# Performance work log

Measured on AMD Instinct MI355X. Metric: run time of the kernel, lower is better.

The kernel has to match this reference:

```python
import jax, jax.numpy as jnp
import numpy as np
from jax import lax

LSTM_UNITS = 64
BATCH = 2048
TIMESTEPS = 1024


def _lstm_cell(x, h, c, W_ih, W_hh, b_ih, b_hh):
    # PyTorch LSTMCell gate order: i, f, g, o
    gates = x @ W_ih.T + b_ih + h @ W_hh.T + b_hh
    i, f, g, o = jnp.split(gates, 4, axis=-1)
    c_new = jax.nn.sigmoid(f) * c + jax.nn.sigmoid(i) * jnp.tanh(g)
    h_new = jax.nn.sigmoid(o) * jnp.tanh(c_new)
    return h_new, c_new


def setup_inputs() -> dict:
    key = jax.random.key(0)
    ks = jax.random.split(key, 9)
    U = LSTM_UNITS
    s0 = 1.0 / np.sqrt(U)  # torch LSTMCell init scale (hidden=64)
    s1 = 1.0  # hidden=1 -> scale 1/sqrt(1)
    inp = {
        "input": jax.random.normal(ks[0], (BATCH, TIMESTEPS), dtype=jnp.float32),
        # c0: LSTMCell(1, 64)
        "W_ih0": jax.random.uniform(ks[1], (4 * U, 1), jnp.float32, -s0, s0),
        "W_hh0": jax.random.uniform(ks[2], (4 * U, U), jnp.float32, -s0, s0),
        "b_ih0": jax.random.uniform(ks[3], (4 * U,), jnp.float32, -s0, s0),
        "b_hh0": jax.random.uniform(ks[4], (4 * U,), jnp.float32, -s0, s0),
        # c1: LSTMCell(64, 1)
        "W_ih1": jax.random.uniform(ks[5], (4, U), jnp.float32, -s1, s1),
        "W_hh1": jax.random.uniform(ks[6], (4, 1), jnp.float32, -s1, s1),
        "b_ih1": jax.random.uniform(ks[7], (4,), jnp.float32, -s1, s1),
        "b_hh1": jax.random.uniform(ks[8], (4,), jnp.float32, -s1, s1),
    }
    return inp


def reference(input, W_ih0, W_hh0, b_ih0, b_hh0, W_ih1, W_hh1, b_ih1, b_hh1):
    B = input.shape[0]
    U = LSTM_UNITS
    dt = input.dtype
    h0 = jnp.zeros((B, U), dt)
    c0 = jnp.zeros((B, U), dt)
    h1 = jnp.zeros((B, 1), dt)
    c1 = jnp.zeros((B, 1), dt)

    def step(carry, x_t):
        h0, c0, h1, c1 = carry
        h0n, c0n = _lstm_cell(x_t, h0, c0, W_ih0, W_hh0, b_ih0, b_hh0)
        # NOTE: the original feeds the CELL state c0n (not h0n) into layer 2
        h1n, c1n = _lstm_cell(c0n, h1, c1, W_ih1, W_hh1, b_ih1, b_hh1)
        # output per step is the cell state of layer 2
        return (h0n, c0n, h1n, c1n), c1n

    xs = input.T[:, :, None]  # (T, B, 1)
    _, ys = lax.scan(step, (h0, c0, h1, c1), xs)  # ys: (T, B, 1)
    return ys[:, :, 0].T  # (B, T)
```

## Files before the change

kernel.cpp:

```cpp
#include <hip/hip_runtime.h>

#define T_STEPS 1024
#define BATCH 2048
#define BTILE 8
#define HS 36

typedef short short8 __attribute__((ext_vector_type(8)));
typedef float f32x4 __attribute__((ext_vector_type(4)));
typedef float f32x2 __attribute__((ext_vector_type(2)));

__device__ __forceinline__ float fast_rcp(float x) {
#if __has_builtin(__builtin_amdgcn_rcpf)
    return __builtin_amdgcn_rcpf(x);
#else
    return 1.0f / x;
#endif
}

__device__ __forceinline__ float fast_exp2(float x) {
#if __has_builtin(__builtin_amdgcn_exp2f)
    return __builtin_amdgcn_exp2f(x);
#else
    return exp2f(x);
#endif
}

__device__ __forceinline__ float sigf(float x) {
    return fast_rcp(1.0f + fast_exp2(-1.44269504f * x));
}

__device__ __forceinline__ f32x2 sigf2(f32x2 v) {
    f32x2 t = v * (-1.44269504f);
    f32x2 e = {fast_exp2(t[0]), fast_exp2(t[1])};
    e = e + 1.0f;
    return f32x2{fast_rcp(e[0]), fast_rcp(e[1])};
}

__device__ __forceinline__ float tanh_fast(float x) {
    float e = fast_exp2(2.88539008f * x);
    return 1.0f - 2.0f * fast_rcp(e + 1.0f);
}

__device__ __forceinline__ f32x2 tanh2(f32x2 v) {
    f32x2 t = v * 2.88539008f;
    f32x2 e = {fast_exp2(t[0]), fast_exp2(t[1])};
    e = e + 1.0f;
    f32x2 r = {fast_rcp(e[0]), fast_rcp(e[1])};
    return f32x2{1.0f, 1.0f} - 2.0f * r;
}

__device__ __forceinline__ unsigned f2bf(float x) {
    unsigned u = __float_as_uint(x);
    unsigned r = u + 0x7FFFu + ((u >> 16) & 1u);
    return r >> 16;
}
__device__ __forceinline__ float bf2f(unsigned b) {
    return __uint_as_float(b << 16);
}

__device__ __forceinline__ unsigned cvt_pk_bf16(float a, float b) {
    unsigned r;
    asm("v_cvt_pk_bf16_f32 %0, %1, %2" : "=v"(r) : "v"(a), "v"(b));
    return r;
}

__device__ __forceinline__ void step_barrier() {
    asm volatile("s_waitcnt lgkmcnt(0)\n\ts_barrier" ::: "memory");
}

__global__ __launch_bounds__(320, 1)
void lstm_v16_kernel(const float* __restrict__ input,
                     const float* __restrict__ W_ih0,
                     const float* __restrict__ W_hh0,
                     const float* __restrict__ b_ih0,
                     const float* __restrict__ b_hh0,
                     const float* __restrict__ W_ih1,
                     const float* __restrict__ W_hh1,
                     const float* __restrict__ b_ih1,
                     const float* __restrict__ b_hh1,
                     float* __restrict__ out)
{
    const int tid = threadIdx.x;
    const int w8  = tid >> 6;
    const int l   = tid & 63;
    const int q16 = l >> 4;
    const int n16 = l & 15;
    const int n8  = l & 7;
    const int hi8 = n16 >> 3;
    const int ua  = 16 * w8 + 4 * q16 + 2 * hi8;
    const int bbase = blockIdx.x * BTILE;

    __shared__ __align__(16) unsigned Hbuf[2][3][16][HS];
    __shared__ float Xb[2][BTILE][65];

    for (int i = tid; i < 2 * 3 * 16 * HS; i += 320)
        reinterpret_cast<unsigned*>(Hbuf)[i] = 0u;

    short8 a1[4][2];
    f32x2 wg2[4], bg2[4];
    if (w8 < 4) {
        #pragma unroll
        for (int g = 0; g < 4; ++g) {
            #pragma unroll
            for (int kt = 0; kt < 2; ++kt) {
                const float* p = W_hh0 + (size_t)(16 * (w8 + 4 * g) + n16) * 64 + kt * 32 + q16 * 8;
                short8 a;
                #pragma unroll
                for (int j = 0; j < 8; ++j) a[j] = (short)f2bf(p[j]);
                a1[g][kt] = a;
            }
        }
        #pragma unroll
        for (int g = 0; g < 4; ++g) {
            int rA = g * 64 + ua;
            int rB = rA + 1;
            wg2[g] = f32x2{W_ih0[rA], W_ih0[rB]};
            bg2[g] = f32x2{b_ih0[rA] + b_hh0[rA], b_ih0[rB] + b_hh0[rB]};
        }
    }

    short8 a2h[2], a2l[2];
    float wh1[4], bb1[4];
    if (w8 == 4) {
        #pragma unroll
        for (int kt = 0; kt < 2; ++kt) {
            short8 ah = {0,0,0,0,0,0,0,0}, al = {0,0,0,0,0,0,0,0};
            if (n16 < 4) {
                const float* p = W_ih1 + (size_t)n16 * 64 + kt * 32 + q16 * 8;
                #pragma unroll
                for (int j = 0; j < 8; ++j) {
                    unsigned hb = f2bf(p[j]);
                    ah[j] = (short)hb;
                    al[j] = (short)f2bf(p[j] - bf2f(hb));
                }
            }
            a2h[kt] = ah; a2l[kt] = al;
        }
        #pragma unroll
        for (int g = 0; g < 4; ++g) { wh1[g] = W_hh1[g]; bb1[g] = b_ih1[g] + b_hh1[g]; }
    }

    const int xr = (tid >> 5) & 7;
    const int xc = tid & 31;
    const float* rowptr = input + (size_t)(bbase + xr) * T_STEPS;
    if (tid < 256) {
        Xb[0][xr][xc]      = rowptr[xc];
        Xb[0][xr][xc + 32] = rowptr[xc + 32];
    }
    float xnA = 0.0f, xnB = 0.0f;
    f32x2 c02 = {0.0f, 0.0f};
    float h1 = 0.0f, c1 = 0.0f;

    __syncthreads();

    int par = 0;
    #pragma unroll 2
    for (int t = 0; t < T_STEPS; ++t) {
        if (w8 < 4) {
            if ((t & 63) == 0 && t + 64 < T_STEPS) {
                xnA = rowptr[t + 64 + xc];
                xnB = rowptr[t + 64 + xc + 32];
            }
            const int cp = (t >> 6) & 1;

            const unsigned* Hrow = &Hbuf[par][0][n16][0];
            short8 hb0 = *reinterpret_cast<const short8*>(Hrow + 4 * q16);
            short8 hb1 = *reinterpret_cast<const short8*>(Hrow + 16 + 4 * q16);

            f32x4 accv[4];
            #pragma unroll
            for (int g = 0; g < 4; ++g) {
                f32x4 z = {0.0f, 0.0f, 0.0f, 0.0f};
                z = __builtin_amdgcn_mfma_f32_16x16x32_bf16(a1[g][0], hb0, z, 0, 0, 0);
                z = __builtin_amdgcn_mfma_f32_16x16x32_bf16(a1[g][1], hb1, z, 0, 0, 0);
                accv[g] = z;
            }

            float vA[4], vB[4];
            #pragma unroll
            for (int g = 0; g < 4; ++g) {
                int pa = __float_as_int(accv[g][0]);
                pa = __builtin_amdgcn_update_dpp(pa, __float_as_int(accv[g][2]), 0x118, 0xf, 0xC, false);
                int pb = __float_as_int(accv[g][1]);
                pb = __builtin_amdgcn_update_dpp(pb, __float_as_int(accv[g][3]), 0x118, 0xf, 0xC, false);
                vA[g] = __int_as_float(pa);
                vB[g] = __int_as_float(pb);
            }

            float x = Xb[cp][n8][t & 63];
            f32x2 xx = {x, x};
            f32x2 gi = f32x2{vA[0], vB[0]} + (xx * wg2[0] + bg2[0]);
            f32x2 gf = f32x2{vA[1], vB[1]} + (xx * wg2[1] + bg2[1]);
            f32x2 gg = f32x2{vA[2], vB[2]} + (xx * wg2[2] + bg2[2]);
            f32x2 go = f32x2{vA[3], vB[3]} + (xx * wg2[3] + bg2[3]);

            f32x2 si = sigf2(gi);
            f32x2 sf = sigf2(gf);
            f32x2 tg = tanh2(gg);
            f32x2 c0n2 = sf * c02 + si * tg;
            c02 = c0n2;
            f32x2 so = sigf2(go);
            f32x2 th = tanh2(c0n2);
            f32x2 h0n2 = so * th;

            const int widx = 8 * w8 + 2 * q16 + hi8;
            unsigned hword  = cvt_pk_bf16(h0n2[0], h0n2[1]);
            Hbuf[par ^ 1][0][n8][widx] = hword;
            unsigned chword = cvt_pk_bf16(c0n2[0], c0n2[1]);
            float hiA = bf2f(chword & 0xFFFFu);
            float hiB = bf2f(chword >> 16);
            f32x2 lo = c0n2 - f32x2{hiA, hiB};
            unsigned clword = cvt_pk_bf16(lo[0], lo[1]);
            Hbuf[par ^ 1][1][n8][widx] = chword;
            Hbuf[par ^ 1][2][n8][widx] = clword;

            if ((t & 63) == 63 && t + 1 < T_STEPS) {
                Xb[cp ^ 1][xr][xc]      = xnA;
                Xb[cp ^ 1][xr][xc + 32] = xnB;
            }
        } else {
            if (t > 0) {
                const unsigned* Ch = &Hbuf[par][1][n16][0];
                const unsigned* Cl = &Hbuf[par][2][n16][0];
                short8 ch0 = *reinterpret_cast<const short8*>(Ch + 4 * q16);
                short8 ch1 = *reinterpret_cast<const short8*>(Ch + 16 + 4 * q16);
                short8 cl0 = *reinterpret_cast<const short8*>(Cl + 4 * q16);
                short8 cl1 = *reinterpret_cast<const short8*>(Cl + 16 + 4 * q16);
                f32x4 zA = {0.0f, 0.0f, 0.0f, 0.0f};
                f32x4 zB = {0.0f, 0.0f, 0.0f, 0.0f};
                zA = __builtin_amdgcn_mfma_f32_16x16x32_bf16(a2h[0], ch0, zA, 0, 0, 0);
                zB = __builtin_amdgcn_mfma_f32_16x16x32_bf16(a2l[1], ch1, zB, 0, 0, 0);
                zA = __builtin_amdgcn_mfma_f32_16x16x32_bf16(a2h[1], ch1, zA, 0, 0, 0);
                zB = __builtin_amdgcn_mfma_f32_16x16x32_bf16(a2h[0], cl0, zB, 0, 0, 0);
                zA = __builtin_amdgcn_mfma_f32_16x16x32_bf16(a2l[0], ch0, zA, 0, 0, 0);
                zB = __builtin_amdgcn_mfma_f32_16x16x32_bf16(a2h[1], cl1, zB, 0, 0, 0);
                f32x4 z = zA + zB;
                if (l < 8) {
                    float gi = z[0] + bb1[0] + h1 * wh1[0];
                    float gf = z[1] + bb1[1] + h1 * wh1[1];
                    float gg = z[2] + bb1[2] + h1 * wh1[2];
                    float go = z[3] + bb1[3] + h1 * wh1[3];
                    float c1n = sigf(gf) * c1 + sigf(gi) * tanh_fast(gg);
                    c1 = c1n;
                    h1 = sigf(go) * tanh_fast(c1n);
                    out[(size_t)(bbase + l) * T_STEPS + (t - 1)] = c1n;
                }
            }
        }

        step_barrier();
        par ^= 1;
    }

    if (w8 == 4) {
        const unsigned* Ch = &Hbuf[par][1][n16][0];
        const unsigned* Cl = &Hbuf[par][2][n16][0];
        short8 ch0 = *reinterpret_cast<const short8*>(Ch + 4 * q16);
        short8 ch1 = *reinterpret_cast<const short8*>(Ch + 16 + 4 * q16);
        short8 cl0 = *reinterpret_cast<const short8*>(Cl + 4 * q16);
        short8 cl1 = *reinterpret_cast<const short8*>(Cl + 16 + 4 * q16);
        f32x4 zA = {0.0f, 0.0f, 0.0f, 0.0f};
        f32x4 zB = {0.0f, 0.0f, 0.0f, 0.0f};
        zA = __builtin_amdgcn_mfma_f32_16x16x32_bf16(a2h[0], ch0, zA, 0, 0, 0);
        zB = __builtin_amdgcn_mfma_f32_16x16x32_bf16(a2l[1], ch1, zB, 0, 0, 0);
        zA = __builtin_amdgcn_mfma_f32_16x16x32_bf16(a2h[1], ch1, zA, 0, 0, 0);
        zB = __builtin_amdgcn_mfma_f32_16x16x32_bf16(a2h[0], cl0, zB, 0, 0, 0);
        zA = __builtin_amdgcn_mfma_f32_16x16x32_bf16(a2l[0], ch0, zA, 0, 0, 0);
        zB = __builtin_amdgcn_mfma_f32_16x16x32_bf16(a2h[1], cl1, zB, 0, 0, 0);
        f32x4 z = zA + zB;
        if (l < 8) {
            float gi = z[0] + bb1[0] + h1 * wh1[0];
            float gf = z[1] + bb1[1] + h1 * wh1[1];
            float gg = z[2] + bb1[2] + h1 * wh1[2];
            float c1n = sigf(gf) * c1 + sigf(gi) * tanh_fast(gg);
            out[(size_t)(bbase + l) * T_STEPS + (T_STEPS - 1)] = c1n;
        }
    }
}

extern "C" void kernel_launch(void* const* d_in, const int* in_sizes, int n_in,
                              void* d_out, int out_size, void* d_ws, size_t ws_size,
                              hipStream_t stream) {
    const float* input = (const float*)d_in[0];
    const float* W_ih0 = (const float*)d_in[1];
    const float* W_hh0 = (const float*)d_in[2];
    const float* b_ih0 = (const float*)d_in[3];
    const float* b_hh0 = (const float*)d_in[4];
    const float* W_ih1 = (const float*)d_in[5];
    const float* W_hh1 = (const float*)d_in[6];
    const float* b_ih1 = (const float*)d_in[7];
    const float* b_hh1 = (const float*)d_in[8];
    float* out = (float*)d_out;

    lstm_v16_kernel<<<dim3(BATCH / BTILE), dim3(320), 0, stream>>>(
        input, W_ih0, W_hh0, b_ih0, b_hh0, W_ih1, W_hh1, b_ih1, b_hh1, out);
}
```

Before: 473.6 us.

## Defer layer-2 cell-state packing to next step and split MFMA accumulation chain

```diff
diff --git a/kernel.cpp b/kernel.cpp
--- a/kernel.cpp
+++ b/kernel.cpp
@@ -69,7 +69,7 @@
 }
 
 __global__ __launch_bounds__(320, 1)
-void lstm_v16_kernel(const float* __restrict__ input,
+void lstm_v18_kernel(const float* __restrict__ input,
                      const float* __restrict__ W_ih0,
                      const float* __restrict__ W_hh0,
                      const float* __restrict__ b_ih0,
@@ -88,6 +88,7 @@
     const int n8  = l & 7;
     const int hi8 = n16 >> 3;
     const int ua  = 16 * w8 + 4 * q16 + 2 * hi8;
+    const int widx = 8 * w8 + 2 * q16 + hi8;
     const int bbase = blockIdx.x * BTILE;
 
     __shared__ __align__(16) unsigned Hbuf[2][3][16][HS];
@@ -149,6 +150,7 @@
     }
     float xnA = 0.0f, xnB = 0.0f;
     f32x2 c02 = {0.0f, 0.0f};
+    f32x2 c_sv = {0.0f, 0.0f};
     float h1 = 0.0f, c1 = 0.0f;
 
     __syncthreads();
@@ -157,6 +159,16 @@
     #pragma unroll 2
     for (int t = 0; t < T_STEPS; ++t) {
         if (w8 < 4) {
+            if (t > 0) {
+                unsigned chword = cvt_pk_bf16(c_sv[0], c_sv[1]);
+                float hiA = bf2f(chword & 0xFFFFu);
+                float hiB = bf2f(chword >> 16);
+                f32x2 lo = c_sv - f32x2{hiA, hiB};
+                unsigned clword = cvt_pk_bf16(lo[0], lo[1]);
+                Hbuf[par ^ 1][1][n8][widx] = chword;
+                Hbuf[par ^ 1][2][n8][widx] = clword;
+            }
+
             if ((t & 63) == 0 && t + 64 < T_STEPS) {
                 xnA = rowptr[t + 64 + xc];
                 xnB = rowptr[t + 64 + xc + 32];
@@ -170,10 +182,10 @@
             f32x4 accv[4];
             #pragma unroll
             for (int g = 0; g < 4; ++g) {
-                f32x4 z = {0.0f, 0.0f, 0.0f, 0.0f};
-                z = __builtin_amdgcn_mfma_f32_16x16x32_bf16(a1[g][0], hb0, z, 0, 0, 0);
-                z = __builtin_amdgcn_mfma_f32_16x16x32_bf16(a1[g][1], hb1, z, 0, 0, 0);
-                accv[g] = z;
+                f32x4 zz = {0.0f, 0.0f, 0.0f, 0.0f};
+                f32x4 z0 = __builtin_amdgcn_mfma_f32_16x16x32_bf16(a1[g][0], hb0, zz, 0, 0, 0);
+                f32x4 z1 = __builtin_amdgcn_mfma_f32_16x16x32_bf16(a1[g][1], hb1, zz, 0, 0, 0);
+                accv[g] = z0 + z1;
             }
 
             float vA[4], vB[4];
@@ -203,23 +215,15 @@
             f32x2 th = tanh2(c0n2);
             f32x2 h0n2 = so * th;
 
-            const int widx = 8 * w8 + 2 * q16 + hi8;
-            unsigned hword  = cvt_pk_bf16(h0n2[0], h0n2[1]);
-            Hbuf[par ^ 1][0][n8][widx] = hword;
-            unsigned chword = cvt_pk_bf16(c0n2[0], c0n2[1]);
-            float hiA = bf2f(chword & 0xFFFFu);
-            float hiB = bf2f(chword >> 16);
-            f32x2 lo = c0n2 - f32x2{hiA, hiB};
-            unsigned clword = cvt_pk_bf16(lo[0], lo[1]);
-            Hbuf[par ^ 1][1][n8][widx] = chword;
-            Hbuf[par ^ 1][2][n8][widx] = clword;
+            Hbuf[par ^ 1][0][n8][widx] = cvt_pk_bf16(h0n2[0], h0n2[1]);
+            c_sv = c0n2;
 
             if ((t & 63) == 63 && t + 1 < T_STEPS) {
                 Xb[cp ^ 1][xr][xc]      = xnA;
                 Xb[cp ^ 1][xr][xc + 32] = xnB;
             }
         } else {
-            if (t > 0) {
+            if (t > 1) {
                 const unsigned* Ch = &Hbuf[par][1][n16][0];
                 const unsigned* Cl = &Hbuf[par][2][n16][0];
                 short8 ch0 = *reinterpret_cast<const short8*>(Ch + 4 * q16);
@@ -243,7 +247,7 @@
                     float c1n = sigf(gf) * c1 + sigf(gi) * tanh_fast(gg);
                     c1 = c1n;
                     h1 = sigf(go) * tanh_fast(c1n);
-                    out[(size_t)(bbase + l) * T_STEPS + (t - 1)] = c1n;
+                    out[(size_t)(bbase + l) * T_STEPS + (t - 2)] = c1n;
                 }
             }
         }
@@ -252,28 +256,45 @@
         par ^= 1;
     }
 
+    if (w8 < 4) {
+        unsigned chword = cvt_pk_bf16(c_sv[0], c_sv[1]);
+        float hiA = bf2f(chword & 0xFFFFu);
+        float hiB = bf2f(chword >> 16);
+        f32x2 lo = c_sv - f32x2{hiA, hiB};
+        unsigned clword = cvt_pk_bf16(lo[0], lo[1]);
+        Hbuf[1][1][n8][widx] = chword;
+        Hbuf[1][2][n8][widx] = clword;
+    }
+    step_barrier();
+
     if (w8 == 4) {
-        const unsigned* Ch = &Hbuf[par][1][n16][0];
-        const unsigned* Cl = &Hbuf[par][2][n16][0];
-        short8 ch0 = *reinterpret_cast<const short8*>(Ch + 4 * q16);
-        short8 ch1 = *reinterpret_cast<const short8*>(Ch + 16 + 4 * q16);
-        short8 cl0 = *reinterpret_cast<const short8*>(Cl + 4 * q16);
-        short8 cl1 = *reinterpret_cast<const short8*>(Cl + 16 + 4 * q16);
-        f32x4 zA = {0.0f, 0.0f, 0.0f, 0.0f};
-        f32x4 zB = {0.0f, 0.0f, 0.0f, 0.0f};
-        zA = __builtin_amdgcn_mfma_f32_16x16x32_bf16(a2h[0], ch0, zA, 0, 0, 0);
-        zB = __builtin_amdgcn_mfma_f32_16x16x32_bf16(a2l[1], ch1, zB, 0, 0, 0);
-        zA = __builtin_amdgcn_mfma_f32_16x16x32_bf16(a2h[1], ch1, zA, 0, 0, 0);
-        zB = __builtin_amdgcn_mfma_f32_16x16x32_bf16(a2h[0], cl0, zB, 0, 0, 0);
-        zA = __builtin_amdgcn_mfma_f32_16x16x32_bf16(a2l[0], ch0, zA, 0, 0, 0);
-        zB = __builtin_amdgcn_mfma_f32_16x16x32_bf16(a2h[1], cl1, zB, 0, 0, 0);
-        f32x4 z = zA + zB;
-        if (l < 8) {
-            float gi = z[0] + bb1[0] + h1 * wh1[0];
-            float gf = z[1] + bb1[1] + h1 * wh1[1];
-            float gg = z[2] + bb1[2] + h1 * wh1[2];
-            float c1n = sigf(gf) * c1 + sigf(gi) * tanh_fast(gg);
-            out[(size_t)(bbase + l) * T_STEPS + (T_STEPS - 1)] = c1n;
+        #pragma unroll
+        for (int eb = 0; eb < 2; ++eb) {
+            const unsigned* Ch = &Hbuf[eb][1][n16][0];
+            const unsigned* Cl = &Hbuf[eb][2][n16][0];
+            short8 ch0 = *reinterpret_cast<const short8*>(Ch + 4 * q16);
+            short8 ch1 = *reinterpret_cast<const short8*>(Ch + 16 + 4 * q16);
+            short8 cl0 = *reinterpret_cast<const short8*>(Cl + 4 * q16);
+            short8 cl1 = *reinterpret_cast<const short8*>(Cl + 16 + 4 * q16);
+            f32x4 zA = {0.0f, 0.0f, 0.0f, 0.0f};
+            f32x4 zB = {0.0f, 0.0f, 0.0f, 0.0f};
+            zA = __builtin_amdgcn_mfma_f32_16x16x32_bf16(a2h[0], ch0, zA, 0, 0, 0);
+            zB = __builtin_amdgcn_mfma_f32_16x16x32_bf16(a2l[1], ch1, zB, 0, 0, 0);
+            zA = __builtin_amdgcn_mfma_f32_16x16x32_bf16(a2h[1], ch1, zA, 0, 0, 0);
+            zB = __builtin_amdgcn_mfma_f32_16x16x32_bf16(a2h[0], cl0, zB, 0, 0, 0);
+            zA = __builtin_amdgcn_mfma_f32_16x16x32_bf16(a2l[0], ch0, zA, 0, 0, 0);
+            zB = __builtin_amdgcn_mfma_f32_16x16x32_bf16(a2h[1], cl1, zB, 0, 0, 0);
+            f32x4 z = zA + zB;
+            if (l < 8) {
+                float gi = z[0] + bb1[0] + h1 * wh1[0];
+                float gf = z[1] + bb1[1] + h1 * wh1[1];
+                float gg = z[2] + bb1[2] + h1 * wh1[2];
+                float go = z[3] + bb1[3] + h1 * wh1[3];
+                float c1n = sigf(gf) * c1 + sigf(gi) * tanh_fast(gg);
+                c1 = c1n;
+                h1 = sigf(go) * tanh_fast(c1n);
+                out[(size_t)(bbase + l) * T_STEPS + (T_STEPS - 2 + eb)] = c1n;
+            }
         }
     }
 }
@@ -292,6 +313,6 @@
     const float* b_hh1 = (const float*)d_in[8];
     float* out = (float*)d_out;
 
-    lstm_v16_kernel<<<dim3(BATCH / BTILE), dim3(320), 0, stream>>>(
+    lstm_v18_kernel<<<dim3(BATCH / BTILE), dim3(320), 0, stream>>>(
         input, W_ih0, W_hh0, b_ih0, b_hh0, W_ih1, W_hh1, b_ih1, b_hh1, out);
 }
```

After: 509.6 us. 1.08x slower.
